# Optimization experiments

Measured on AMD Instinct MI355X. Metric: run time of the kernel, lower is better.

The kernel has to match this reference:

```python
import jax, jax.numpy as jnp
import numpy as np

B, LATENT, U_DIM, NUM_PROD, NUM_INJ, HID = 4096, 128, 24, 16, 8, 200
ZU = LATENT + U_DIM  # 152


def setup_inputs() -> dict:
    key = jax.random.key(0)
    ks = jax.random.split(key, 24)

    def w(k, shape, fan_in):
        return jax.random.normal(k, shape, jnp.float32) * (1.0 / np.sqrt(fan_in))

    inp = {
        "zt": jax.random.normal(ks[0], (B, LATENT), jnp.float32),
        "dt": jax.random.uniform(ks[1], (B, 1), jnp.float32),
        "ut": jax.random.uniform(ks[2], (B, U_DIM), jnp.float32),
        # trans_encoder: (latent+1) -> 200 -> 200 -> latent, ReLU between
        "We1": w(ks[3], (HID, LATENT + 1), LATENT + 1), "be1": jnp.zeros((HID,), jnp.float32),
        "We2": w(ks[4], (HID, HID), HID),               "be2": jnp.zeros((HID,), jnp.float32),
        "We3": w(ks[5], (LATENT, HID), HID),            "be3": jnp.zeros((LATENT,), jnp.float32),
        # At / Bt projections
        "WA": w(ks[6], (LATENT * LATENT, LATENT), LATENT), "bA": jnp.zeros((LATENT * LATENT,), jnp.float32),
        "WB": w(ks[7], (LATENT * U_DIM, LATENT), LATENT),  "bB": jnp.zeros((LATENT * U_DIM,), jnp.float32),
        # per-well heads, stacked over head dim h: zu(152) -> 64 -> 64 -> 2
        "Wh1": w(ks[8], (NUM_PROD, 64, ZU), ZU),  "bh1": jnp.zeros((NUM_PROD, 64), jnp.float32),
        "Wh2": w(ks[9], (NUM_PROD, 64, 64), 64),  "bh2": jnp.zeros((NUM_PROD, 64), jnp.float32),
        "Wh3": w(ks[10], (NUM_PROD, 2, 64), 64),  "bh3": jnp.zeros((NUM_PROD, 2), jnp.float32),
        # injector head: zu -> num_inj
        "Wi": w(ks[11], (NUM_INJ, ZU), ZU), "bi": jnp.zeros((NUM_INJ,), jnp.float32),
    }
    return inp


def _forward(zt, dt, ut, We1, be1, We2, be2, We3, be3, WA, bA, WB, bB,
             Wh1, bh1, Wh2, bh2, Wh3, bh3, Wi, bi):
    b = zt.shape[0]
    # encoder on [zt, dt]
    x = jnp.concatenate([zt, dt], axis=-1)                      # [B, latent+1]
    h = jax.nn.relu(x @ We1.T + be1)
    h = jax.nn.relu(h @ We2.T + be2)
    hz = h @ We3.T + be3                                        # [B, latent]
    # state transition matrices
    At = (hz @ WA.T + bA).reshape(b, LATENT, LATENT)            # [B, L, L]
    Bt = (hz @ WB.T + bB).reshape(b, LATENT, U_DIM)             # [B, L, U]
    ut_dt = ut * dt                                             # [B, U]
    zt1 = jnp.einsum('bij,bj->bi', At, zt) + jnp.einsum('biu,bu->bi', Bt, ut_dt)
    # per-well heads on zu, fused as batched GEMMs over head dim h
    zu = jnp.concatenate([zt1, ut], axis=-1)                    # [B, 152]
    g = jax.nn.relu(jnp.einsum('bz,hoz->bho', zu, Wh1) + bh1)   # [B, H, 64]
    g = jax.nn.relu(jnp.einsum('bho,hpo->bhp', g, Wh2) + bh2)   # [B, H, 64]
    wells = (jnp.einsum('bho,hpo->bhp', g, Wh3) + bh3).reshape(b, NUM_PROD * 2)
    inj = zu @ Wi.T + bi                                        # [B, num_inj]
    yt1 = jnp.concatenate([wells, inj], axis=-1)                # [B, 40]
    return zt1, yt1


def reference(zt, dt, ut, We1, be1, We2, be2, We3, be3, WA, bA, WB, bB,
              Wh1, bh1, Wh2, bh2, Wh3, bh3, Wi, bi):
    return _forward(zt, dt, ut, We1, be1, We2, be2, We3, be3, WA, bA, WB, bB,
                    Wh1, bh1, Wh2, bh2, Wh3, bh3, Wi, bi)
```

## Files before the change

### kernel.cpp

```cpp
#include <hip/hip_runtime.h>
#include <hip/hip_bf16.h>


#define NB   4096
#define LAT  128
#define UD   24
#define HIDN 200
#define ZUD  152
#define JPD  152

#define GT_OFF      0u
#define GB_OFF      2490368u
#define HZ_OFF      2509824u
#define PART_OFF    3034112u
#define PART_STRIDE 524288u
#define WH1P_OFF    7228416u
#define WH2P_OFF    7392256u
#define WH3P_OFF    7457792u

typedef __attribute__((ext_vector_type(8))) short short8_t;
typedef __attribute__((ext_vector_type(4))) float f32x4;

union FragU { short8_t s; unsigned short u[8]; };
union Frag2 { short8_t s; __hip_bfloat162 h2[4]; };

__device__ __forceinline__ unsigned short bf16_rne(float x) {
  const unsigned u = __float_as_uint(x);
  return (unsigned short)((u + 0x7FFFu + ((u >> 16) & 1u)) >> 16);
}
__device__ __forceinline__ unsigned short bf16_hi(float x) {
  return (unsigned short)(__float_as_uint(x) >> 16);
}
__device__ __forceinline__ unsigned short bf16_lo(float x) {
  const float hif = __uint_as_float(__float_as_uint(x) & 0xFFFF0000u);
  return bf16_rne(x - hif);
}

#define MFMA_BF16(A, B, C) __builtin_amdgcn_mfma_f32_16x16x32_bf16((A), (B), (C), 0, 0, 0)

__global__ __launch_bounds__(256, 2)
void prep_kernel(const float* __restrict__ WA, const float* __restrict__ bA,
                 const float* __restrict__ WB, const float* __restrict__ bB,
                 unsigned short* __restrict__ GtU, float* __restrict__ Gb,
                 const float* __restrict__ zt, const float* __restrict__ dt,
                 const float* __restrict__ We1, const float* __restrict__ be1,
                 const float* __restrict__ We2, const float* __restrict__ be2,
                 const float* __restrict__ We3, const float* __restrict__ be3,
                 float* __restrict__ hz,
                 const float* __restrict__ Wh1, const float* __restrict__ Wh2,
                 const float* __restrict__ Wh3,
                 short8_t* __restrict__ WH1P, short8_t* __restrict__ WH2P,
                 short8_t* __restrict__ WH3P) {
  __shared__ union {
    float tile[128][132];
    struct { float xs[8][132]; float h1[8][200]; float h2[8][200]; } e;
    struct { float w1[64][152]; float w2[64][64]; float w3[2][64]; } hp;
  } sh;
  const int t = threadIdx.x;

  if (blockIdx.x < 152) {
    const int jp = blockIdx.x;
    const bool isA = (jp < LAT);
    const float* __restrict__ src = isA ? WA : WB;
    const int mul = isA ? LAT : UD;
    const int sub = isA ? jp : (jp - LAT);

    for (int idx = t; idx < 4096; idx += 256) {
      const int i = idx >> 5, c4 = (idx & 31) << 2;
      *(float4*)(&sh.tile[i][c4]) = *(const float4*)(src + (size_t)(i * mul + sub) * 128 + c4);
    }
    __syncthreads();

    if (t < 128) {
      const float* __restrict__ bsrc = isA ? bA : bB;
      Gb[(jp << 7) + t] = bsrc[t * mul + sub];
    }

    short8_t* __restrict__ G8 = (short8_t*)GtU;
#pragma unroll
    for (int q = 0; q < 16; ++q) {
      const int c   = (q << 8) + t;
      const int l   = c & 63;
      const int spl = (c >> 6) & 1;
      const int n   = (c >> 7) & 7;
      const int ksq = (c >> 10) & 3;
      const int icol = (n << 4) + (l & 15);
      const int k0   = (ksq << 5) + ((l >> 4) << 3);
      FragU fr;
#pragma unroll
      for (int j = 0; j < 8; ++j) {
        const float g = sh.tile[icol][k0 + j];
        fr.u[j] = spl ? bf16_lo(g) : bf16_hi(g);
      }
      G8[(size_t)jp * 4096 + c] = fr.s;
    }
    return;
  }

  if (blockIdx.x >= 664) {
    const int h = blockIdx.x - 664;
    for (int idx = t; idx < 2432; idx += 256) {
      const int r = idx / 38, c4 = (idx - r * 38) << 2;
      *(float4*)(&sh.hp.w1[r][c4]) = *(const float4*)(Wh1 + ((size_t)h * 64 + r) * ZUD + c4);
    }
    for (int idx = t; idx < 1024; idx += 256) {
      const int r = idx >> 4, c4 = (idx & 15) << 2;
      *(float4*)(&sh.hp.w2[r][c4]) = *(const float4*)(Wh2 + ((size_t)h * 64 + r) * 64 + c4);
    }
    if (t < 32) {
      const int r = t >> 4, c4 = (t & 15) << 2;
      *(float4*)(&sh.hp.w3[r][c4]) = *(const float4*)(Wh3 + ((size_t)h * 2 + r) * 64 + c4);
    }
    __syncthreads();

    for (int c = t; c < 2560; c += 256) {
      const int l = c & 63, spl = (c >> 6) & 1, nt = (c >> 7) & 3, ks = c >> 9;
      const int col = (nt << 4) + (l & 15);
      const int k0  = (ks << 5) + ((l >> 4) << 3);
      FragU fr;
#pragma unroll
      for (int j = 0; j < 8; ++j) {
        const int k = k0 + j;
        const float v = (k < ZUD) ? sh.hp.w1[col][k] : 0.f;
        fr.u[j] = spl ? bf16_lo(v) : bf16_hi(v);
      }
      WH1P[(size_t)h * 2560 + c] = fr.s;
    }
    for (int c = t; c < 1024; c += 256) {
      const int l = c & 63, spl = (c >> 6) & 1, nt = (c >> 7) & 3, ks = (c >> 9) & 1;
      const int col = (nt << 4) + (l & 15);
      const int k0  = (ks << 5) + ((l >> 4) << 3);
      FragU fr;
#pragma unroll
      for (int j = 0; j < 8; ++j) {
        const float v = sh.hp.w2[col][k0 + j];
        fr.u[j] = spl ? bf16_lo(v) : bf16_hi(v);
      }
      WH2P[(size_t)h * 1024 + c] = fr.s;
    }
    for (int c = t; c < 256; c += 256) {
      const int l = c & 63, spl = (c >> 6) & 1, ks = (c >> 7) & 1;
      const int col = l & 15;
      const int k0  = (ks << 5) + ((l >> 4) << 3);
      FragU fr;
#pragma unroll
      for (int j = 0; j < 8; ++j) {
        const float v = (col < 2) ? sh.hp.w3[col][k0 + j] : 0.f;
        fr.u[j] = spl ? bf16_lo(v) : bf16_hi(v);
      }
      WH3P[(size_t)h * 256 + c] = fr.s;
    }
    return;
  }

  const int b0 = (blockIdx.x - 152) * 8;

  for (int idx = t; idx < 8 * 129; idx += 256) {
    const int r = idx / 129, c = idx - r * 129;
    sh.e.xs[r][c] = (c < LAT) ? zt[(size_t)(b0 + r) * LAT + c] : dt[b0 + r];
  }
  __syncthreads();

  if (t < HIDN) {
    const float* __restrict__ w = We1 + t * 129;
    float acc[8];
    const float bias = be1[t];
#pragma unroll
    for (int r = 0; r < 8; ++r) acc[r] = bias;
    for (int c = 0; c < 128; c += 4) {
      const float w0 = w[c], w1 = w[c + 1], w2 = w[c + 2], w3 = w[c + 3];
#pragma unroll
      for (int r = 0; r < 8; ++r) {
        const float4 xv = *(const float4*)(&sh.e.xs[r][c]);
        acc[r] += xv.x * w0 + xv.y * w1 + xv.z * w2 + xv.w * w3;
      }
    }
    const float wl = w[128];
#pragma unroll
    for (int r = 0; r < 8; ++r) sh.e.h1[r][t] = fmaxf(fmaf(sh.e.xs[r][128], wl, acc[r]), 0.f);
  }
  __syncthreads();

  if (t < HIDN) {
    const float* __restrict__ w = We2 + t * HIDN;
    float acc[8];
    const float bias = be2[t];
#pragma unroll
    for (int r = 0; r < 8; ++r) acc[r] = bias;
    for (int c = 0; c < HIDN; c += 4) {
      const float4 wv = *(const float4*)(w + c);
#pragma unroll
      for (int r = 0; r < 8; ++r) {
        const float4 hv = *(const float4*)(&sh.e.h1[r][c]);
        acc[r] += hv.x * wv.x + hv.y * wv.y + hv.z * wv.z + hv.w * wv.w;
      }
    }
#pragma unroll
    for (int r = 0; r < 8; ++r) sh.e.h2[r][t] = fmaxf(acc[r], 0.f);
  }
  __syncthreads();

  if (t < LAT) {
    const float* __restrict__ w = We3 + t * HIDN;
    float acc[8];
    const float bias = be3[t];
#pragma unroll
    for (int r = 0; r < 8; ++r) acc[r] = bias;
    for (int c = 0; c < HIDN; c += 4) {
      const float4 wv = *(const float4*)(w + c);
#pragma unroll
      for (int r = 0; r < 8; ++r) {
        const float4 hv = *(const float4*)(&sh.e.h2[r][c]);
        acc[r] += hv.x * wv.x + hv.y * wv.y + hv.z * wv.z + hv.w * wv.w;
      }
    }
#pragma unroll
    for (int r = 0; r < 8; ++r) hz[(size_t)(b0 + r) * LAT + t] = acc[r];
  }
}

#define GBODY(JP, B00, B01, B10, B11, NJP)                                      \
  {                                                                             \
    const int jp_ = (JP);                                                       \
    const float w0_ = wtile[(rw << 5) + lr][jp_];                               \
    const float w1_ = wtile[(rw << 5) + 16 + lr][jp_];                          \
    Frag2 p0_, p1_;                                                             \
    _Pragma("unroll")                                                           \
    for (int jq = 0; jq < 4; ++jq) {                                            \
      p0_.h2[jq] = __float22bfloat162_rn(                                       \
          make_float2(w0_ * hzr0[2 * jq], w0_ * hzr0[2 * jq + 1]));             \
      p1_.h2[jq] = __float22bfloat162_rn(                                       \
          make_float2(w1_ * hzr1[2 * jq], w1_ * hzr1[2 * jq + 1]));             \
    }                                                                           \
    acc00 = MFMA_BF16(p0_.s, B00, acc00);                                       \
    acc00 = MFMA_BF16(p0_.s, B01, acc00);                                       \
    acc01 = MFMA_BF16(p0_.s, B10, acc01);                                       \
    acc01 = MFMA_BF16(p0_.s, B11, acc01);                                       \
    acc10 = MFMA_BF16(p1_.s, B00, acc10);                                       \
    acc10 = MFMA_BF16(p1_.s, B01, acc10);                                       \
    acc11 = MFMA_BF16(p1_.s, B10, acc11);                                       \
    acc11 = MFMA_BF16(p1_.s, B11, acc11);                                       \
    const size_t nb_ = (size_t)(NJP) * 4096;                                    \
    B00 = G8[nb_ + c00]; B01 = G8[nb_ + c01];                                   \
    B10 = G8[nb_ + c10]; B11 = G8[nb_ + c11];                                   \
  }

__global__ __launch_bounds__(512, 4)
void gemm_mfma_kernel(const float* __restrict__ zt, const float* __restrict__ dt,
                      const float* __restrict__ ut,
                      const unsigned short* __restrict__ GtU,
                      const float* __restrict__ Gb,
                      const float* __restrict__ hz, float* __restrict__ part) {
  __shared__ float wtile[64][156];
  const int t  = threadIdx.x;
  const int l  = t & 63;
  const int w  = t >> 6;
  const int rw = w & 1, cw = w >> 1;
  const int bid   = blockIdx.x;
  const int combo = bid & 7;
  const int ks    = combo & 3;
  const int jph   = combo >> 2;
  const int b0    = (bid >> 3) << 6;
  const int lr  = l & 15, lg = l >> 4;
  const int j0  = jph * 76;

  for (int idx = t; idx < 2048; idx += 512) {
    const int r = idx >> 5, c4 = (idx & 31) << 2;
    *(float4*)(&wtile[r][c4]) = *(const float4*)(zt + (((size_t)(b0 + r)) << 7) + c4);
  }
  for (int idx = t; idx < 384; idx += 512) {
    const int r = idx / 6, u4 = (idx - r * 6) << 2;
    float4 v = *(const float4*)(ut + (size_t)(b0 + r) * UD + u4);
    const float s = dt[b0 + r];
    v.x *= s; v.y *= s; v.z *= s; v.w *= s;
    *(float4*)(&wtile[r][LAT + u4]) = v;
  }
  __syncthreads();

  const int kk = (ks << 5) + (lg << 3);
  float hzr0[8], hzr1[8];
  {
    const float* __restrict__ hp0 = hz + (((size_t)(b0 + (rw << 5) + lr)) << 7) + kk;
    const float* __restrict__ hp1 = hz + (((size_t)(b0 + (rw << 5) + 16 + lr)) << 7) + kk;
    const float4 a0 = *(const float4*)hp0, b0v = *(const float4*)(hp0 + 4);
    const float4 a1 = *(const float4*)hp1, b1v = *(const float4*)(hp1 + 4);
    hzr0[0]=a0.x; hzr0[1]=a0.y; hzr0[2]=a0.z; hzr0[3]=a0.w;
    hzr0[4]=b0v.x; hzr0[5]=b0v.y; hzr0[6]=b0v.z; hzr0[7]=b0v.w;
    hzr1[0]=a1.x; hzr1[1]=a1.y; hzr1[2]=a1.z; hzr1[3]=a1.w;
    hzr1[4]=b1v.x; hzr1[5]=b1v.y; hzr1[6]=b1v.z; hzr1[7]=b1v.w;
  }

  const short8_t* __restrict__ G8 = (const short8_t*)GtU;
  const int n0 = (cw << 1), n1 = (cw << 1) + 1;
  const int c00 = ((((ks << 3) + n0) << 1) + 0) * 64 + l;
  const int c01 = ((((ks << 3) + n0) << 1) + 1) * 64 + l;
  const int c10 = ((((ks << 3) + n1) << 1) + 0) * 64 + l;
  const int c11 = ((((ks << 3) + n1) << 1) + 1) * 64 + l;

  f32x4 acc00 = {0.f,0.f,0.f,0.f}, acc01 = {0.f,0.f,0.f,0.f};
  f32x4 acc10 = {0.f,0.f,0.f,0.f}, acc11 = {0.f,0.f,0.f,0.f};

  short8_t A0 = G8[(size_t)(j0+0)*4096 + c00], A1 = G8[(size_t)(j0+0)*4096 + c01],
           A2 = G8[(size_t)(j0+0)*4096 + c10], A3 = G8[(size_t)(j0+0)*4096 + c11];
  short8_t Bv0 = G8[(size_t)(j0+1)*4096 + c00], Bv1 = G8[(size_t)(j0+1)*4096 + c01],
           Bv2 = G8[(size_t)(j0+1)*4096 + c10], Bv3 = G8[(size_t)(j0+1)*4096 + c11];
  short8_t C0 = G8[(size_t)(j0+2)*4096 + c00], C1 = G8[(size_t)(j0+2)*4096 + c01],
           C2 = G8[(size_t)(j0+2)*4096 + c10], C3 = G8[(size_t)(j0+2)*4096 + c11];
  short8_t D0 = G8[(size_t)(j0+3)*4096 + c00], D1 = G8[(size_t)(j0+3)*4096 + c01],
           D2 = G8[(size_t)(j0+3)*4096 + c10], D3 = G8[(size_t)(j0+3)*4096 + c11];

  const int jend = j0 + 76;
  for (int jp = j0; jp < jend; jp += 4) {
    const int n4 = (jp + 4 < jend) ? jp + 4 : jend - 1;
    const int n5 = (jp + 5 < jend) ? jp + 5 : jend - 1;
    const int n6 = (jp + 6 < jend) ? jp + 6 : jend - 1;
    const int n7 = (jp + 7 < jend) ? jp + 7 : jend - 1;
    GBODY(jp + 0, A0, A1, A2, A3, n4);
    GBODY(jp + 1, Bv0, Bv1, Bv2, Bv3, n5);
    GBODY(jp + 2, C0, C1, C2, C3, n6);
    GBODY(jp + 3, D0, D1, D2, D3, n7);
  }

  {
    const int jb0 = combo * 19;
    for (int jp = jb0; jp < jb0 + 19; ++jp) {
      const float gb0 = Gb[(jp << 7) + (cw << 5) + lr];
      const float gb1 = Gb[(jp << 7) + (cw << 5) + 16 + lr];
#pragma unroll
      for (int r = 0; r < 4; ++r) {
        const float wv0 = wtile[(rw << 5) + (lg << 2) + r][jp];
        const float wv1 = wtile[(rw << 5) + 16 + (lg << 2) + r][jp];
        acc00[r] += wv0 * gb0; acc01[r] += wv0 * gb1;
        acc10[r] += wv1 * gb0; acc11[r] += wv1 * gb1;
      }
    }
  }

  float* __restrict__ dst = part + (size_t)combo * PART_STRIDE + (((size_t)b0) << 7);
  const int colb = (cw << 5) + lr;
#pragma unroll
  for (int r = 0; r < 4; ++r) {
    const int row0 = (rw << 5) + (lg << 2) + r;
    const int row1 = row0 + 16;
    dst[((size_t)row0 << 7) + colb]      = acc00[r];
    dst[((size_t)row0 << 7) + colb + 16] = acc01[r];
    dst[((size_t)row1 << 7) + colb]      = acc10[r];
    dst[((size_t)row1 << 7) + colb + 16] = acc11[r];
  }
}

__global__ __launch_bounds__(512, 2)
void heads_kernel(const float* __restrict__ ut, const float* __restrict__ part,
                  const short8_t* __restrict__ WH1P, const float* __restrict__ bh1,
                  const short8_t* __restrict__ WH2P, const float* __restrict__ bh2,
                  const short8_t* __restrict__ WH3P, const float* __restrict__ bh3,
                  const float* __restrict__ Wi, const float* __restrict__ bi,
                  float* __restrict__ out) {
  __shared__ float    zuf[64][156];
  __shared__ short8_t zua[2560];
  __shared__ short8_t g1a[1024];
  __shared__ short8_t g2a[1024];
  const int t  = threadIdx.x;
  const int l  = t & 63;
  const int w  = t >> 6;
  const int wm = w >> 1, wn = w & 1;
  const int mb = blockIdx.x >> 2;
  const int hg = blockIdx.x & 3;
  const int b0 = mb << 6;
  float* __restrict__ zt1_out = out;
  float* __restrict__ yt1_out = out + (size_t)NB * LAT;

  for (int idx = t; idx < 2048; idx += 512) {
    const int r = idx >> 5, c4 = (idx & 31) << 2;
    const size_t off = (((size_t)(b0 + r)) << 7) + c4;
    float4 s = *(const float4*)(part + off);
#pragma unroll
    for (int q = 1; q < 8; ++q) {
      const float4 v = *(const float4*)(part + (size_t)q * PART_STRIDE + off);
      s.x += v.x; s.y += v.y; s.z += v.z; s.w += v.w;
    }
    *(float4*)(&zuf[r][c4]) = s;
    if (hg == 0) *(float4*)(zt1_out + off) = s;
  }
  for (int idx = t; idx < 384; idx += 512) {
    const int r = idx / 6, u4 = (idx - r * 6) << 2;
    *(float4*)(&zuf[r][LAT + u4]) = *(const float4*)(ut + (size_t)(b0 + r) * UD + u4);
  }
  __syncthreads();

  for (int c = t; c < 2560; c += 512) {
    const int cl = c & 63;
    const int q  = c >> 6;
    const int spl = q & 1;
    const int q2  = q >> 1;
    const int ks  = q2 % 5;
    const int mt  = q2 / 5;
    const int row = (mt << 4) + (cl & 15);
    const int k0  = (ks << 5) + ((cl >> 4) << 3);
    FragU fr;
#pragma unroll
    for (int j = 0; j < 8; ++j) {
      const int k = k0 + j;
      const float v = (k < ZUD) ? zuf[row][k] : 0.f;
      fr.u[j] = spl ? bf16_lo(v) : bf16_hi(v);
    }
    zua[c] = fr.s;
  }
  __syncthreads();

  short8_t Ahi[5], Alo[5];
#pragma unroll
  for (int ks = 0; ks < 5; ++ks) {
    Ahi[ks] = zua[(((wm * 5 + ks) << 1) + 0) * 64 + l];
    Alo[ks] = zua[(((wm * 5 + ks) << 1) + 1) * 64 + l];
  }

  unsigned short* __restrict__ g1s = (unsigned short*)g1a;
  unsigned short* __restrict__ g2s = (unsigned short*)g2a;
  const int lq = l >> 4;

  for (int hc = 0; hc < 4; ++hc) {
    const int hh = (hg << 2) + hc;

    const short8_t* __restrict__ W1 = WH1P + (size_t)hh * 2560;
    short8_t b1h[5][2], b1l[5][2];
#pragma unroll
    for (int ks = 0; ks < 5; ++ks)
#pragma unroll
      for (int nt = 0; nt < 2; ++nt) {
        const int ntg = (wn << 1) + nt;
        b1h[ks][nt] = W1[(((ks << 2) + ntg) * 2 + 0) * 64 + l];
        b1l[ks][nt] = W1[(((ks << 2) + ntg) * 2 + 1) * 64 + l];
      }
    f32x4 a1[2] = {{0.f,0.f,0.f,0.f},{0.f,0.f,0.f,0.f}};
#pragma unroll
    for (int ks = 0; ks < 5; ++ks)
#pragma unroll
      for (int nt = 0; nt < 2; ++nt) {
        a1[nt] = MFMA_BF16(Ahi[ks], b1h[ks][nt], a1[nt]);
        a1[nt] = MFMA_BF16(Alo[ks], b1h[ks][nt], a1[nt]);
        a1[nt] = MFMA_BF16(Ahi[ks], b1l[ks][nt], a1[nt]);
      }
#pragma unroll
    for (int nt = 0; nt < 2; ++nt) {
      const int C = (wn << 5) + (nt << 4) + (l & 15);
      const float bv = bh1[(hh << 6) + C];
      const int chunkbase = (((wm << 1) + (C >> 5)) << 1);
      const int lp = (lq << 2) | (((C >> 3) & 3) << 4);
#pragma unroll
      for (int r = 0; r < 4; ++r) {
        const float v = fmaxf(a1[nt][r] + bv, 0.f);
        const int lpr = (lp + r) | (lp & 0x30);
        const int lane2 = ((lq << 2) + r) | ((((C >> 3) & 3)) << 4);
        const int ch_hi = (chunkbase + 0) * 64 + lane2;
        const int ch_lo = (chunkbase + 1) * 64 + lane2;
        g1s[(ch_hi << 3) + (C & 7)] = bf16_hi(v);
        g1s[(ch_lo << 3) + (C & 7)] = bf16_lo(v);
        (void)lpr;
      }
    }
    __syncthreads();

    const short8_t* __restrict__ W2 = WH2P + (size_t)hh * 1024;
    short8_t A2h[2], A2l[2];
#pragma unroll
    for (int ks = 0; ks < 2; ++ks) {
      A2h[ks] = g1a[(((wm << 1) + ks) * 2 + 0) * 64 + l];
      A2l[ks] = g1a[(((wm << 1) + ks) * 2 + 1) * 64 + l];
    }
    f32x4 a2[2] = {{0.f,0.f,0.f,0.f},{0.f,0.f,0.f,0.f}};
#pragma unroll
    for (int ks = 0; ks < 2; ++ks)
#pragma unroll
      for (int nt = 0; nt < 2; ++nt) {
        const int ntg = (wn << 1) + nt;
        const short8_t bh = W2[(((ks << 2) + ntg) * 2 + 0) * 64 + l];
        const short8_t bl = W2[(((ks << 2) + ntg) * 2 + 1) * 64 + l];
        a2[nt] = MFMA_BF16(A2h[ks], bh, a2[nt]);
        a2[nt] = MFMA_BF16(A2l[ks], bh, a2[nt]);
        a2[nt] = MFMA_BF16(A2h[ks], bl, a2[nt]);
      }
#pragma unroll
    for (int nt = 0; nt < 2; ++nt) {
      const int C = (wn << 5) + (nt << 4) + (l & 15);
      const float bv = bh2[(hh << 6) + C];
      const int chunkbase = (((wm << 1) + (C >> 5)) << 1);
#pragma unroll
      for (int r = 0; r < 4; ++r) {
        const float v = fmaxf(a2[nt][r] + bv, 0.f);
        const int lane2 = ((lq << 2) + r) | ((((C >> 3) & 3)) << 4);
        g2s[(((chunkbase + 0) * 64 + lane2) << 3) + (C & 7)] = bf16_hi(v);
        g2s[(((chunkbase + 1) * 64 + lane2) << 3) + (C & 7)] = bf16_lo(v);
      }
    }
    __syncthreads();

    if (wn == 0) {
      const short8_t* __restrict__ W3 = WH3P + (size_t)hh * 256;
      f32x4 a3 = {0.f,0.f,0.f,0.f};
#pragma unroll
      for (int ks = 0; ks < 2; ++ks) {
        const short8_t Ah = g2a[(((wm << 1) + ks) * 2 + 0) * 64 + l];
        const short8_t Al = g2a[(((wm << 1) + ks) * 2 + 1) * 64 + l];
        const short8_t bh = W3[((ks << 1) + 0) * 64 + l];
        const short8_t bl = W3[((ks << 1) + 1) * 64 + l];
        a3 = MFMA_BF16(Ah, bh, a3);
        a3 = MFMA_BF16(Al, bh, a3);
        a3 = MFMA_BF16(Ah, bl, a3);
      }
      if ((l & 15) < 2) {
        const int col = l & 15;
        const float bv = bh3[(hh << 1) + col];
#pragma unroll
        for (int r = 0; r < 4; ++r) {
          const int R = (wm << 4) + (lq << 2) + r;
          yt1_out[(size_t)(b0 + R) * 40 + (hh << 1) + col] = a3[r] + bv;
        }
      }
    }
  }

  if (hg == 3) {
    const int r  = t >> 3, io = t & 7;
    const float4* __restrict__ wrow = (const float4*)(Wi + (size_t)io * ZUD);
    const float4* __restrict__ zr   = (const float4*)(&zuf[r][0]);
    float a0 = 0, a1 = 0, a2 = 0, a3 = 0;
#pragma unroll
    for (int cc = 0; cc < 38; ++cc) {
      const float4 wv = wrow[cc];
      const float4 zv = zr[cc];
      a0 = fmaf(wv.x, zv.x, a0); a1 = fmaf(wv.y, zv.y, a1);
      a2 = fmaf(wv.z, zv.z, a2); a3 = fmaf(wv.w, zv.w, a3);
    }
    yt1_out[(size_t)(b0 + r) * 40 + 32 + io] = a0 + a1 + a2 + a3 + bi[io];
  }
}

extern "C" void kernel_launch(void* const* d_in, const int* in_sizes, int n_in,
                              void* d_out, int out_size, void* d_ws, size_t ws_size,
                              hipStream_t stream) {
  const float* zt  = (const float*)d_in[0];
  const float* dt  = (const float*)d_in[1];
  const float* ut  = (const float*)d_in[2];
  const float* We1 = (const float*)d_in[3];
  const float* be1 = (const float*)d_in[4];
  const float* We2 = (const float*)d_in[5];
  const float* be2 = (const float*)d_in[6];
  const float* We3 = (const float*)d_in[7];
  const float* be3 = (const float*)d_in[8];
  const float* WA  = (const float*)d_in[9];
  const float* bA  = (const float*)d_in[10];
  const float* WB  = (const float*)d_in[11];
  const float* bB  = (const float*)d_in[12];
  const float* Wh1 = (const float*)d_in[13];
  const float* bh1 = (const float*)d_in[14];
  const float* Wh2 = (const float*)d_in[15];
  const float* bh2 = (const float*)d_in[16];
  const float* Wh3 = (const float*)d_in[17];
  const float* bh3 = (const float*)d_in[18];
  const float* Wi  = (const float*)d_in[19];
  const float* bi  = (const float*)d_in[20];

  float* ws = (float*)d_ws;
  unsigned short* GtU = (unsigned short*)(ws + GT_OFF);
  float* Gb   = ws + GB_OFF;
  float* hz   = ws + HZ_OFF;
  float* part = ws + PART_OFF;
  short8_t* WH1P = (short8_t*)(ws + WH1P_OFF);
  short8_t* WH2P = (short8_t*)(ws + WH2P_OFF);
  short8_t* WH3P = (short8_t*)(ws + WH3P_OFF);
  float* out  = (float*)d_out;

  hipLaunchKernelGGL(prep_kernel, dim3(152 + NB / 8 + 16), dim3(256), 0, stream,
                     WA, bA, WB, bB, GtU, Gb,
                     zt, dt, We1, be1, We2, be2, We3, be3, hz,
                     Wh1, Wh2, Wh3, WH1P, WH2P, WH3P);
  hipLaunchKernelGGL(gemm_mfma_kernel, dim3(512), dim3(512), 0, stream,
                     zt, dt, ut, GtU, Gb, hz, part);
  hipLaunchKernelGGL(heads_kernel, dim3(256), dim3(512), 0, stream,
                     ut, part, WH1P, bh1, WH2P, bh2, WH3P, bh3, Wi, bi, out);
}
```

Measured before the change: 231.9 us.

## Shrink shared memory in prep and heads kernels to raise occupancy

The prep kernel now stages the WA/WB slice in four 32-row passes instead of one 128-row tile, and head-weight packing reads global memory directly instead of going through LDS. The heads kernel drops the packed zu staging buffer and builds the bf16 hi/lo A fragments straight from the fp32 LDS rows. Launch bounds rise to allow more resident blocks per CU. The aim is to cut LDS footprint and one barrier so more waves can hide latency, at the cost of extra barriers in prep and uncoalesced global reads for the head weights.

```diff
diff --git a/kernel.cpp b/kernel.cpp
--- a/kernel.cpp
+++ b/kernel.cpp
@@ -38,7 +38,7 @@
 
 #define MFMA_BF16(A, B, C) __builtin_amdgcn_mfma_f32_16x16x32_bf16((A), (B), (C), 0, 0, 0)
 
-__global__ __launch_bounds__(256, 2)
+__global__ __launch_bounds__(256, 5)
 void prep_kernel(const float* __restrict__ WA, const float* __restrict__ bA,
                  const float* __restrict__ WB, const float* __restrict__ bB,
                  unsigned short* __restrict__ GtU, float* __restrict__ Gb,
@@ -52,9 +52,8 @@
                  short8_t* __restrict__ WH1P, short8_t* __restrict__ WH2P,
                  short8_t* __restrict__ WH3P) {
   __shared__ union {
-    float tile[128][132];
+    float tile32[32][132];
     struct { float xs[8][132]; float h1[8][200]; float h2[8][200]; } e;
-    struct { float w1[64][152]; float w2[64][64]; float w3[2][64]; } hp;
   } sh;
   const int t = threadIdx.x;
 
@@ -64,64 +63,56 @@
     const float* __restrict__ src = isA ? WA : WB;
     const int mul = isA ? LAT : UD;
     const int sub = isA ? jp : (jp - LAT);
-
-    for (int idx = t; idx < 4096; idx += 256) {
-      const int i = idx >> 5, c4 = (idx & 31) << 2;
-      *(float4*)(&sh.tile[i][c4]) = *(const float4*)(src + (size_t)(i * mul + sub) * 128 + c4);
-    }
-    __syncthreads();
+    short8_t* __restrict__ G8 = (short8_t*)GtU;
 
     if (t < 128) {
       const float* __restrict__ bsrc = isA ? bA : bB;
       Gb[(jp << 7) + t] = bsrc[t * mul + sub];
     }
 
-    short8_t* __restrict__ G8 = (short8_t*)GtU;
-#pragma unroll
-    for (int q = 0; q < 16; ++q) {
-      const int c   = (q << 8) + t;
-      const int l   = c & 63;
-      const int spl = (c >> 6) & 1;
-      const int n   = (c >> 7) & 7;
-      const int ksq = (c >> 10) & 3;
-      const int icol = (n << 4) + (l & 15);
-      const int k0   = (ksq << 5) + ((l >> 4) << 3);
-      FragU fr;
-#pragma unroll
-      for (int j = 0; j < 8; ++j) {
-        const float g = sh.tile[icol][k0 + j];
-        fr.u[j] = spl ? bf16_lo(g) : bf16_hi(g);
-      }
-      G8[(size_t)jp * 4096 + c] = fr.s;
+    for (int p = 0; p < 4; ++p) {
+      for (int idx = t; idx < 1024; idx += 256) {
+        const int i = idx >> 5, c4 = (idx & 31) << 2;
+        *(float4*)(&sh.tile32[i][c4]) =
+            *(const float4*)(src + (size_t)(((p << 5) + i) * mul + sub) * 128 + c4);
+      }
+      __syncthreads();
+#pragma unroll
+      for (int q = 0; q < 4; ++q) {
+        const int cc  = (q << 8) + t;
+        const int l   = cc & 63;
+        const int spl = (cc >> 6) & 1;
+        const int nloc = (cc >> 7) & 1;
+        const int ksq  = (cc >> 8) & 3;
+        const int n    = (p << 1) + nloc;
+        const int icl  = (nloc << 4) + (l & 15);
+        const int k0   = (ksq << 5) + ((l >> 4) << 3);
+        FragU fr;
+#pragma unroll
+        for (int j = 0; j < 8; ++j) {
+          const float g = sh.tile32[icl][k0 + j];
+          fr.u[j] = spl ? bf16_lo(g) : bf16_hi(g);
+        }
+        const int c = ((((ksq << 3) + n) << 1) + spl) * 64 + l;
+        G8[(size_t)jp * 4096 + c] = fr.s;
+      }
+      __syncthreads();
     }
     return;
   }
 
   if (blockIdx.x >= 664) {
     const int h = blockIdx.x - 664;
-    for (int idx = t; idx < 2432; idx += 256) {
-      const int r = idx / 38, c4 = (idx - r * 38) << 2;
-      *(float4*)(&sh.hp.w1[r][c4]) = *(const float4*)(Wh1 + ((size_t)h * 64 + r) * ZUD + c4);
-    }
-    for (int idx = t; idx < 1024; idx += 256) {
-      const int r = idx >> 4, c4 = (idx & 15) << 2;
-      *(float4*)(&sh.hp.w2[r][c4]) = *(const float4*)(Wh2 + ((size_t)h * 64 + r) * 64 + c4);
-    }
-    if (t < 32) {
-      const int r = t >> 4, c4 = (t & 15) << 2;
-      *(float4*)(&sh.hp.w3[r][c4]) = *(const float4*)(Wh3 + ((size_t)h * 2 + r) * 64 + c4);
-    }
-    __syncthreads();
-
     for (int c = t; c < 2560; c += 256) {
       const int l = c & 63, spl = (c >> 6) & 1, nt = (c >> 7) & 3, ks = c >> 9;
       const int col = (nt << 4) + (l & 15);
       const int k0  = (ks << 5) + ((l >> 4) << 3);
+      const float* __restrict__ wr = Wh1 + ((size_t)h * 64 + col) * ZUD;
       FragU fr;
 #pragma unroll
       for (int j = 0; j < 8; ++j) {
         const int k = k0 + j;
-        const float v = (k < ZUD) ? sh.hp.w1[col][k] : 0.f;
+        const float v = (k < ZUD) ? wr[k] : 0.f;
         fr.u[j] = spl ? bf16_lo(v) : bf16_hi(v);
       }
       WH1P[(size_t)h * 2560 + c] = fr.s;
@@ -130,10 +121,11 @@
       const int l = c & 63, spl = (c >> 6) & 1, nt = (c >> 7) & 3, ks = (c >> 9) & 1;
       const int col = (nt << 4) + (l & 15);
       const int k0  = (ks << 5) + ((l >> 4) << 3);
+      const float* __restrict__ wr = Wh2 + ((size_t)h * 64 + col) * 64 + k0;
       FragU fr;
 #pragma unroll
       for (int j = 0; j < 8; ++j) {
-        const float v = sh.hp.w2[col][k0 + j];
+        const float v = wr[j];
         fr.u[j] = spl ? bf16_lo(v) : bf16_hi(v);
       }
       WH2P[(size_t)h * 1024 + c] = fr.s;
@@ -145,7 +137,7 @@
       FragU fr;
 #pragma unroll
       for (int j = 0; j < 8; ++j) {
-        const float v = (col < 2) ? sh.hp.w3[col][k0 + j] : 0.f;
+        const float v = (col < 2) ? Wh3[((size_t)h * 2 + col) * 64 + k0 + j] : 0.f;
         fr.u[j] = spl ? bf16_lo(v) : bf16_hi(v);
       }
       WH3P[(size_t)h * 256 + c] = fr.s;
@@ -349,7 +341,7 @@
   }
 }
 
-__global__ __launch_bounds__(512, 2)
+__global__ __launch_bounds__(512, 4)
 void heads_kernel(const float* __restrict__ ut, const float* __restrict__ part,
                   const short8_t* __restrict__ WH1P, const float* __restrict__ bh1,
                   const short8_t* __restrict__ WH2P, const float* __restrict__ bh2,
@@ -357,7 +349,6 @@
                   const float* __restrict__ Wi, const float* __restrict__ bi,
                   float* __restrict__ out) {
   __shared__ float    zuf[64][156];
-  __shared__ short8_t zua[2560];
   __shared__ short8_t g1a[1024];
   __shared__ short8_t g2a[1024];
   const int t  = threadIdx.x;
@@ -388,31 +379,25 @@
   }
   __syncthreads();
 
-  for (int c = t; c < 2560; c += 512) {
-    const int cl = c & 63;
-    const int q  = c >> 6;
-    const int spl = q & 1;
-    const int q2  = q >> 1;
-    const int ks  = q2 % 5;
-    const int mt  = q2 / 5;
-    const int row = (mt << 4) + (cl & 15);
-    const int k0  = (ks << 5) + ((cl >> 4) << 3);
-    FragU fr;
-#pragma unroll
-    for (int j = 0; j < 8; ++j) {
-      const int k = k0 + j;
-      const float v = (k < ZUD) ? zuf[row][k] : 0.f;
-      fr.u[j] = spl ? bf16_lo(v) : bf16_hi(v);
-    }
-    zua[c] = fr.s;
-  }
-  __syncthreads();
-
   short8_t Ahi[5], Alo[5];
-#pragma unroll
-  for (int ks = 0; ks < 5; ++ks) {
-    Ahi[ks] = zua[(((wm * 5 + ks) << 1) + 0) * 64 + l];
-    Alo[ks] = zua[(((wm * 5 + ks) << 1) + 1) * 64 + l];
+  {
+    const int arow = (wm << 4) + (l & 15);
+#pragma unroll
+    for (int ks = 0; ks < 5; ++ks) {
+      const int k0 = (ks << 5) + ((l >> 4) << 3);
+      FragU fh, fl;
+      if (k0 < ZUD) {
+        const float4 va = *(const float4*)(&zuf[arow][k0]);
+        const float4 vb = *(const float4*)(&zuf[arow][k0 + 4]);
+        const float vv[8] = {va.x, va.y, va.z, va.w, vb.x, vb.y, vb.z, vb.w};
+#pragma unroll
+        for (int j = 0; j < 8; ++j) { fh.u[j] = bf16_hi(vv[j]); fl.u[j] = bf16_lo(vv[j]); }
+      } else {
+#pragma unroll
+        for (int j = 0; j < 8; ++j) { fh.u[j] = 0; fl.u[j] = 0; }
+      }
+      Ahi[ks] = fh.s; Alo[ks] = fl.s;
+    }
   }
 
   unsigned short* __restrict__ g1s = (unsigned short*)g1a;
@@ -446,17 +431,12 @@
       const int C = (wn << 5) + (nt << 4) + (l & 15);
       const float bv = bh1[(hh << 6) + C];
       const int chunkbase = (((wm << 1) + (C >> 5)) << 1);
-      const int lp = (lq << 2) | (((C >> 3) & 3) << 4);
 #pragma unroll
       for (int r = 0; r < 4; ++r) {
         const float v = fmaxf(a1[nt][r] + bv, 0.f);
-        const int lpr = (lp + r) | (lp & 0x30);
         const int lane2 = ((lq << 2) + r) | ((((C >> 3) & 3)) << 4);
-        const int ch_hi = (chunkbase + 0) * 64 + lane2;
-        const int ch_lo = (chunkbase + 1) * 64 + lane2;
-        g1s[(ch_hi << 3) + (C & 7)] = bf16_hi(v);
-        g1s[(ch_lo << 3) + (C & 7)] = bf16_lo(v);
-        (void)lpr;
+        g1s[(((chunkbase + 0) * 64 + lane2) << 3) + (C & 7)] = bf16_hi(v);
+        g1s[(((chunkbase + 1) * 64 + lane2) << 3) + (C & 7)] = bf16_lo(v);
       }
     }
     __syncthreads();
```

New measurement: 234.7 us. No clear change (+1.2%).
